# Kernel optimization log

Hardware: AMD Instinct MI355X
Metric: run time of the kernel (lower is better)

Reference implementation:

```python
import jax, jax.numpy as jnp
import numpy as np

HIDDEN = 1024

def _cat_linear(x, W, b, cat_ids):
    # x: (B,T,Din), W: (C,Din,Dout), b: (C,Dout)
    return jnp.einsum('bti,bio->bto', x, W[cat_ids]) + b[cat_ids][:, None, :]

def _sinusoidal(timesteps, dim):
    # timesteps: (B,T) int -> (B,T,dim)
    t = timesteps.astype(jnp.float32)
    half = dim // 2
    exponent = -jnp.arange(half, dtype=jnp.float32) * (jnp.log(10000.0) / half)
    freqs = t[..., None] * jnp.exp(exponent)
    return jnp.concatenate([jnp.sin(freqs), jnp.cos(freqs)], axis=-1)

def setup_inputs() -> dict:
    key = jax.random.key(0)
    ks = jax.random.split(key, 8)
    B, T, A, H, C = 64, 64, 64, HIDDEN, 16
    actions = jax.random.normal(ks[0], (B, T, A), dtype=jnp.float32)
    timesteps = jax.random.randint(ks[1], (B,), 0, 1000)
    cat_ids = jax.random.randint(ks[2], (B,), 0, C)
    W1 = 0.02 * jax.random.normal(ks[3], (C, A, H), dtype=jnp.float32)
    b1 = jnp.zeros((C, H), dtype=jnp.float32)
    W2 = 0.02 * jax.random.normal(ks[4], (C, 2 * H, H), dtype=jnp.float32)
    b2 = jnp.zeros((C, H), dtype=jnp.float32)
    W3 = 0.02 * jax.random.normal(ks[5], (C, H, H), dtype=jnp.float32)
    b3 = jnp.zeros((C, H), dtype=jnp.float32)
    return {"actions": actions, "timesteps": timesteps, "cat_ids": cat_ids,
            "W1": W1, "b1": b1, "W2": W2, "b2": b2, "W3": W3, "b3": b3}

def reference(actions, timesteps, cat_ids, W1, b1, W2, b2, W3, b3):
    B, T, _ = actions.shape
    ts = jnp.broadcast_to(timesteps[:, None], (B, T))  # (B,T)
    a_emb = _cat_linear(actions, W1, b1, cat_ids)        # (B,T,H)
    tau = _sinusoidal(ts, HIDDEN).astype(a_emb.dtype)    # (B,T,H)
    x = jnp.concatenate([a_emb, tau], axis=-1)           # (B,T,2H)
    h = _cat_linear(x, W2, b2, cat_ids)
    h = h * jax.nn.sigmoid(h)                            # swish
    return _cat_linear(h, W3, b3, cat_ids)               # (B,T,H)
```

## Files before the change

kernel.cpp:

```cpp
#include <hip/hip_runtime.h>
#include <math.h>


typedef short bf16x8 __attribute__((ext_vector_type(8)));
typedef float floatx4 __attribute__((ext_vector_type(4)));

__device__ inline short f2bf(float f) {
  union { float f; unsigned u; } v; v.f = f;
  unsigned u = v.u;
  return (short)(((u + 0x7fffu + ((u >> 16) & 1u)) >> 16) & 0xffffu);
}

__device__ __forceinline__ unsigned cvtpk(float a, float b) {
  unsigned r;
  asm("v_cvt_pk_bf16_f32 %0, %1, %2" : "=v"(r) : "v"(a), "v"(b));
  return r;
}

template<int IMM>
__device__ __forceinline__ void gdw(float& d, unsigned voff, unsigned long long base) {
  asm volatile("global_load_dword %0, %1, %2 offset:%3"
               : "=v"(d) : "v"(voff), "s"(base), "n"(IMM) : "memory");
}
template<int IMM>
__device__ __forceinline__ void gdx4(floatx4& d, unsigned voff, unsigned long long base) {
  asm volatile("global_load_dwordx4 %0, %1, %2 offset:%3"
               : "=v"(d) : "v"(voff), "s"(base), "n"(IMM) : "memory");
}
template<int N>
__device__ __forceinline__ void vm_wait() {
  asm volatile("s_waitcnt vmcnt(%0)" :: "n"(N) : "memory");
}

#define ISSUE_W(WBUF) do {                                                   \
    _Pragma("unroll")                                                        \
    for (int j = 0; j < 8; ++j) {                                            \
      gdw<0 >(WBUF[j],     vW[j], Wq);                                       \
      gdw<64>(WBUF[8 + j], vW[j], Wq);                                       \
    }                                                                        \
    Wq += 32ull * 1024 * 4;                                                  \
  } while (0)

#define ISSUE_A(ABUF) do {                                                   \
    _Pragma("unroll")                                                        \
    for (int mt = 0; mt < 8; ++mt) {                                         \
      if constexpr (A_F32) {                                                 \
        gdx4<0 >(ABUF[2 * mt],     vA[mt], Aq);                              \
        gdx4<16>(ABUF[2 * mt + 1], vA[mt], Aq);                              \
      } else {                                                               \
        gdx4<0>(ABUF[mt], vA[mt], Aq);                                       \
      }                                                                      \
    }                                                                        \
    Aq += 32ull * AB;                                                        \
  } while (0)

#define KSTEP(VM, AIN, AOUT, WIN, DO_A, DO_W) do {                           \
    vm_wait<VM>();                                                           \
    __builtin_amdgcn_sched_barrier(0);                                       \
    union { bf16x8 v; unsigned u[4]; } wb0, wb1;                             \
    _Pragma("unroll")                                                        \
    for (int jj = 0; jj < 4; ++jj) {                                         \
      wb0.u[jj] = cvtpk(WIN[2 * jj],     WIN[2 * jj + 1]);                   \
      wb1.u[jj] = cvtpk(WIN[8 + 2 * jj], WIN[8 + 2 * jj + 1]);               \
    }                                                                        \
    bf16x8 af[8];                                                            \
    _Pragma("unroll")                                                        \
    for (int mt = 0; mt < 8; ++mt) {                                         \
      if constexpr (A_F32) {                                                 \
        union { bf16x8 v; unsigned u[4]; } t;                                \
        floatx4 x0 = AIN[2 * mt], x1 = AIN[2 * mt + 1];                      \
        t.u[0] = cvtpk(x0[0], x0[1]); t.u[1] = cvtpk(x0[2], x0[3]);          \
        t.u[2] = cvtpk(x1[0], x1[1]); t.u[3] = cvtpk(x1[2], x1[3]);          \
        af[mt] = t.v;                                                        \
      } else {                                                               \
        union { floatx4 f; bf16x8 v; } t; t.f = AIN[mt]; af[mt] = t.v;       \
      }                                                                      \
    }                                                                        \
    __builtin_amdgcn_sched_barrier(0);                                       \
    if (DO_A) ISSUE_A(AOUT);                                                 \
    if (DO_W) ISSUE_W(WIN);                                                  \
    _Pragma("unroll")                                                        \
    for (int mt = 0; mt < 8; ++mt) {                                         \
      acc[mt][0] = __builtin_amdgcn_mfma_f32_16x16x32_bf16(af[mt], wb0.v, acc[mt][0], 0, 0, 0); \
      acc[mt][1] = __builtin_amdgcn_mfma_f32_16x16x32_bf16(af[mt], wb1.v, acc[mt][1], 0, 0, 0); \
    }                                                                        \
  } while (0)

template<int K, bool A_F32, bool SWISH, bool OUT_BF16, bool TAU>
__global__ __launch_bounds__(128, 2) void gemm_kernel(
    const void* __restrict__ Aall, int lda,
    const float* __restrict__ Wall,
    const float* __restrict__ bias,
    const int* __restrict__ cat_ids,
    void* __restrict__ Out, int ldo,
    const int* __restrict__ ts)
{
  constexpr int NCOL = 1024;
  constexpr int KT = K / 32;
  constexpr int AB = A_F32 ? 4 : 2;
  static_assert(KT >= 2 && ((KT - 2) % 2 == 0), "K must be multiple of 64");
  (void)ts;

  __shared__ int s_b[80], s_c[80], s_np;

  const int tid = threadIdx.x;
  if (tid < 80) { s_b[tid] = -1; s_c[tid] = 0; }
  __syncthreads();
  if (tid < 64) {
    const int myc = cat_ids[tid];
    int rank = 0, pst = 0, tot = 0;
    #pragma unroll
    for (int cc = 0; cc < 16; ++cc) {
      unsigned long long m = __ballot(myc == cc);
      const int cnt = __popcll(m);
      const int pc  = 2 * ((cnt + 1) >> 1);
      if (cc < myc)  pst += pc;
      if (cc == myc) rank = __popcll(m & ((1ull << tid) - 1ull));
      tot += pc;
    }
    const int slot = pst + rank;
    s_b[slot] = tid;
    s_c[slot] = myc;
    if (tid == 0) s_np = tot >> 1;
  }
  __syncthreads();

  const int e = blockIdx.y;
  if (e >= s_np) return;
  const int b0v = __builtin_amdgcn_readfirstlane(s_b[2 * e]);
  int b1        = __builtin_amdgcn_readfirstlane(s_b[2 * e + 1]);
  const int c   = __builtin_amdgcn_readfirstlane(s_c[2 * e]);
  const bool st1 = (b1 >= 0);
  if (!st1) b1 = b0v;

  const int wave = tid >> 6, lane = tid & 63;
  const int quad = lane >> 4, l16 = lane & 15;
  const int ns = blockIdx.x * 64;
  const int wcol = ns + wave * 32;

  const unsigned wqoff = (unsigned)__builtin_amdgcn_readfirstlane(
      (int)(((unsigned)c * (unsigned)K * NCOL + (unsigned)wcol) * 4u));
  unsigned long long Wq = (unsigned long long)Wall + wqoff;
  unsigned long long Aq = (unsigned long long)Aall;

  unsigned vW[8];
  #pragma unroll
  for (int j = 0; j < 8; ++j)
    vW[j] = (unsigned)((quad * 8 + j) * (NCOL * 4) + l16 * 4);

  unsigned vA[8];
  #pragma unroll
  for (int mt = 0; mt < 8; ++mt) {
    const int pr = mt * 16 + l16;
    const int batch = (pr < 64) ? b0v : b1;
    const int row = batch * 64 + (pr & 63);
    vA[mt] = (unsigned)(row * lda * AB + quad * 8 * AB);
  }

  float wA[16], wB[16];
  floatx4 aBuf0[A_F32 ? 16 : 8];
  floatx4 aBuf1[A_F32 ? 1 : 8];

  floatx4 acc[8][2];
  #pragma unroll
  for (int mt = 0; mt < 8; ++mt) {
    acc[mt][0] = (floatx4){0.f, 0.f, 0.f, 0.f};
    acc[mt][1] = (floatx4){0.f, 0.f, 0.f, 0.f};
  }

  ISSUE_W(wA);
  ISSUE_A(aBuf0);
  ISSUE_W(wB);

  if constexpr (A_F32) {
    #pragma unroll 1
    for (int s = 0; s + 2 < KT; s += 2) {
      KSTEP(16, aBuf0, aBuf0, wA, true, true);
      KSTEP(16, aBuf0, aBuf0, wB, true, true);
    }
    KSTEP(16, aBuf0, aBuf0, wA, true, false);
    KSTEP(0,  aBuf0, aBuf0, wB, false, false);
  } else {
    #pragma unroll 1
    for (int s = 0; s + 2 < KT; s += 2) {
      KSTEP(16, aBuf0, aBuf1, wA, true, true);
      KSTEP(16, aBuf1, aBuf0, wB, true, true);
    }
    KSTEP(16, aBuf0, aBuf1, wA, true, false);
    KSTEP(0,  aBuf1, aBuf1, wB, false, false);
  }

  #pragma unroll
  for (int nt = 0; nt < 2; ++nt) {
    const int col = wcol + nt * 16 + l16;
    const float bv = bias[(size_t)c * NCOL + col];
    #pragma unroll
    for (int mt = 0; mt < 8; ++mt) {
      const int prb = mt * 16 + quad * 4;
      const int batch = (prb < 64) ? b0v : b1;
      const bool do_store = (prb < 64) || st1;
      #pragma unroll
      for (int r = 0; r < 4; ++r) {
        const int row = batch * 64 + ((prb + r) & 63);
        float v = acc[mt][nt][r] + bv;
        if constexpr (SWISH) v = v / (1.f + __expf(-v));
        if (do_store) {
          if constexpr (OUT_BF16)
            ((short*)Out)[(size_t)row * ldo + col] = f2bf(v);
          else
            ((float*)Out)[(size_t)row * ldo + col] = v;
        }
      }
    }
  }

  if constexpr (TAU) {
    const float t0  = (float)ts[b0v];
    const float t1v = (float)ts[b1];
    const int ic = ns + (tid & 63);
    const int hi = ic & 511;
    const float ef = __expf(-(float)hi * 0.017988946039015980f);
    float v0, v1;
    if (ic < 512) { v0 = sinf(t0 * ef); v1 = sinf(t1v * ef); }
    else          { v0 = cosf(t0 * ef); v1 = cosf(t1v * ef); }
    const short q0 = f2bf(v0), q1 = f2bf(v1);
    short* xp = (short*)Out;
    const int r0 = tid >> 6;
    #pragma unroll 4
    for (int rr = 0; rr < 32; ++rr) {
      const int rl = r0 + 2 * rr;
      xp[(size_t)(b0v * 64 + rl) * ldo + 1024 + ic] = q0;
      if (st1) xp[(size_t)(b1 * 64 + rl) * ldo + 1024 + ic] = q1;
    }
  }
}

extern "C" void kernel_launch(void* const* d_in, const int* in_sizes, int n_in,
                              void* d_out, int out_size, void* d_ws, size_t ws_size,
                              hipStream_t stream) {
  const float* actions   = (const float*)d_in[0];
  const int*   timesteps = (const int*)  d_in[1];
  const int*   cat_ids   = (const int*)  d_in[2];
  const float* W1 = (const float*)d_in[3];
  const float* B1 = (const float*)d_in[4];
  const float* W2 = (const float*)d_in[5];
  const float* B2 = (const float*)d_in[6];
  const float* W3 = (const float*)d_in[7];
  const float* B3 = (const float*)d_in[8];

  short* x = (short*)d_ws;
  short* h = x + (size_t)64 * 64 * 2048;

  dim3 grid(16, 40), blk(128);

  gemm_kernel<64, true, false, true, true><<<grid, blk, 0, stream>>>(
      (const void*)actions, 64, W1, B1, cat_ids, (void*)x, 2048, timesteps);
  gemm_kernel<2048, false, true, true, false><<<grid, blk, 0, stream>>>(
      (const void*)x, 2048, W2, B2, cat_ids, (void*)h, 1024, nullptr);
  gemm_kernel<1024, false, false, false, false><<<grid, blk, 0, stream>>>(
      (const void*)h, 1024, W3, B3, cat_ids, d_out, 1024, nullptr);
}
```

Baseline: 406.8 us.

## Replace hand-pipelined asm loads with plain single-wave loop, smaller blocks

Removes the inline-asm global loads, manual vmcnt waits and double-buffered software pipeline, and replaces them with a plain C++ k-loop (unroll 2) that loads weights and activations directly. Blocks shrink to one wave of 64 threads covering 32 columns, so the grid doubles in x and the LDS/syncthreads category sort becomes a pure ballot-based computation. The hardware bf16 pack instruction is swapped for software rounding. This simplifies the code and raises block count, but gives up explicit load/compute overlap and adds ALU work for conversion.

Result: slower. 534.2 us (+31.3%).

```diff
diff --git a/kernel.cpp b/kernel.cpp
--- a/kernel.cpp
+++ b/kernel.cpp
@@ -11,83 +11,15 @@
   return (short)(((u + 0x7fffu + ((u >> 16) & 1u)) >> 16) & 0xffffu);
 }
 
-__device__ __forceinline__ unsigned cvtpk(float a, float b) {
-  unsigned r;
-  asm("v_cvt_pk_bf16_f32 %0, %1, %2" : "=v"(r) : "v"(a), "v"(b));
-  return r;
+__device__ __forceinline__ unsigned pk2(float a, float b) {
+  union { float f; unsigned u; } x, y; x.f = a; y.f = b;
+  unsigned ua = (x.u + 0x7fffu + ((x.u >> 16) & 1u)) >> 16;
+  unsigned ub = (y.u + 0x7fffu + ((y.u >> 16) & 1u)) >> 16;
+  return (ua & 0xffffu) | (ub << 16);
 }
 
-template<int IMM>
-__device__ __forceinline__ void gdw(float& d, unsigned voff, unsigned long long base) {
-  asm volatile("global_load_dword %0, %1, %2 offset:%3"
-               : "=v"(d) : "v"(voff), "s"(base), "n"(IMM) : "memory");
-}
-template<int IMM>
-__device__ __forceinline__ void gdx4(floatx4& d, unsigned voff, unsigned long long base) {
-  asm volatile("global_load_dwordx4 %0, %1, %2 offset:%3"
-               : "=v"(d) : "v"(voff), "s"(base), "n"(IMM) : "memory");
-}
-template<int N>
-__device__ __forceinline__ void vm_wait() {
-  asm volatile("s_waitcnt vmcnt(%0)" :: "n"(N) : "memory");
-}
-
-#define ISSUE_W(WBUF) do {                                                   \
-    _Pragma("unroll")                                                        \
-    for (int j = 0; j < 8; ++j) {                                            \
-      gdw<0 >(WBUF[j],     vW[j], Wq);                                       \
-      gdw<64>(WBUF[8 + j], vW[j], Wq);                                       \
-    }                                                                        \
-    Wq += 32ull * 1024 * 4;                                                  \
-  } while (0)
-
-#define ISSUE_A(ABUF) do {                                                   \
-    _Pragma("unroll")                                                        \
-    for (int mt = 0; mt < 8; ++mt) {                                         \
-      if constexpr (A_F32) {                                                 \
-        gdx4<0 >(ABUF[2 * mt],     vA[mt], Aq);                              \
-        gdx4<16>(ABUF[2 * mt + 1], vA[mt], Aq);                              \
-      } else {                                                               \
-        gdx4<0>(ABUF[mt], vA[mt], Aq);                                       \
-      }                                                                      \
-    }                                                                        \
-    Aq += 32ull * AB;                                                        \
-  } while (0)
-
-#define KSTEP(VM, AIN, AOUT, WIN, DO_A, DO_W) do {                           \
-    vm_wait<VM>();                                                           \
-    __builtin_amdgcn_sched_barrier(0);                                       \
-    union { bf16x8 v; unsigned u[4]; } wb0, wb1;                             \
-    _Pragma("unroll")                                                        \
-    for (int jj = 0; jj < 4; ++jj) {                                         \
-      wb0.u[jj] = cvtpk(WIN[2 * jj],     WIN[2 * jj + 1]);                   \
-      wb1.u[jj] = cvtpk(WIN[8 + 2 * jj], WIN[8 + 2 * jj + 1]);               \
-    }                                                                        \
-    bf16x8 af[8];                                                            \
-    _Pragma("unroll")                                                        \
-    for (int mt = 0; mt < 8; ++mt) {                                         \
-      if constexpr (A_F32) {                                                 \
-        union { bf16x8 v; unsigned u[4]; } t;                                \
-        floatx4 x0 = AIN[2 * mt], x1 = AIN[2 * mt + 1];                      \
-        t.u[0] = cvtpk(x0[0], x0[1]); t.u[1] = cvtpk(x0[2], x0[3]);          \
-        t.u[2] = cvtpk(x1[0], x1[1]); t.u[3] = cvtpk(x1[2], x1[3]);          \
-        af[mt] = t.v;                                                        \
-      } else {                                                               \
-        union { floatx4 f; bf16x8 v; } t; t.f = AIN[mt]; af[mt] = t.v;       \
-      }                                                                      \
-    }                                                                        \
-    __builtin_amdgcn_sched_barrier(0);                                       \
-    if (DO_A) ISSUE_A(AOUT);                                                 \
-    if (DO_W) ISSUE_W(WIN);                                                  \
-    _Pragma("unroll")                                                        \
-    for (int mt = 0; mt < 8; ++mt) {                                         \
-      acc[mt][0] = __builtin_amdgcn_mfma_f32_16x16x32_bf16(af[mt], wb0.v, acc[mt][0], 0, 0, 0); \
-      acc[mt][1] = __builtin_amdgcn_mfma_f32_16x16x32_bf16(af[mt], wb1.v, acc[mt][1], 0, 0, 0); \
-    }                                                                        \
-  } while (0)
-
 template<int K, bool A_F32, bool SWISH, bool OUT_BF16, bool TAU>
-__global__ __launch_bounds__(128, 2) void gemm_kernel(
+__global__ __launch_bounds__(64, 2) void gemm_kernel(
     const void* __restrict__ Aall, int lda,
     const float* __restrict__ Wall,
     const float* __restrict__ bias,
@@ -97,69 +29,43 @@
 {
   constexpr int NCOL = 1024;
   constexpr int KT = K / 32;
-  constexpr int AB = A_F32 ? 4 : 2;
-  static_assert(KT >= 2 && ((KT - 2) % 2 == 0), "K must be multiple of 64");
   (void)ts;
 
-  __shared__ int s_b[80], s_c[80], s_np;
+  const int lane = threadIdx.x;
+  const int quad = lane >> 4, l16 = lane & 15;
 
-  const int tid = threadIdx.x;
-  if (tid < 80) { s_b[tid] = -1; s_c[tid] = 0; }
-  __syncthreads();
-  if (tid < 64) {
-    const int myc = cat_ids[tid];
-    int rank = 0, pst = 0, tot = 0;
-    #pragma unroll
-    for (int cc = 0; cc < 16; ++cc) {
-      unsigned long long m = __ballot(myc == cc);
-      const int cnt = __popcll(m);
-      const int pc  = 2 * ((cnt + 1) >> 1);
-      if (cc < myc)  pst += pc;
-      if (cc == myc) rank = __popcll(m & ((1ull << tid) - 1ull));
-      tot += pc;
-    }
-    const int slot = pst + rank;
-    s_b[slot] = tid;
-    s_c[slot] = myc;
-    if (tid == 0) s_np = tot >> 1;
+  const int myc = cat_ids[lane];
+  int rank = 0, pst = 0, tot = 0;
+  #pragma unroll
+  for (int cc = 0; cc < 16; ++cc) {
+    const unsigned long long m = __ballot(myc == cc);
+    const int cnt = __popcll(m);
+    const int pc  = 2 * ((cnt + 1) >> 1);
+    if (cc < myc)  pst += pc;
+    if (cc == myc) rank = __popcll(m & ((1ull << lane) - 1ull));
+    tot += pc;
   }
-  __syncthreads();
+  const int slot = pst + rank;
+  const int e = blockIdx.y;
+  if (e >= (tot >> 1)) return;
+  const unsigned long long m0 = __ballot(slot == 2 * e);
+  const unsigned long long m1 = __ballot(slot == 2 * e + 1);
+  const int b0v = __ffsll(m0) - 1;
+  const bool st1 = (m1 != 0ull);
+  const int b1 = st1 ? (__ffsll(m1) - 1) : b0v;
+  const int c = cat_ids[b0v];
 
-  const int e = blockIdx.y;
-  if (e >= s_np) return;
-  const int b0v = __builtin_amdgcn_readfirstlane(s_b[2 * e]);
-  int b1        = __builtin_amdgcn_readfirstlane(s_b[2 * e + 1]);
-  const int c   = __builtin_amdgcn_readfirstlane(s_c[2 * e]);
-  const bool st1 = (b1 >= 0);
-  if (!st1) b1 = b0v;
+  const int ns = blockIdx.x * 32;
 
-  const int wave = tid >> 6, lane = tid & 63;
-  const int quad = lane >> 4, l16 = lane & 15;
-  const int ns = blockIdx.x * 64;
-  const int wcol = ns + wave * 32;
-
-  const unsigned wqoff = (unsigned)__builtin_amdgcn_readfirstlane(
-      (int)(((unsigned)c * (unsigned)K * NCOL + (unsigned)wcol) * 4u));
-  unsigned long long Wq = (unsigned long long)Wall + wqoff;
-  unsigned long long Aq = (unsigned long long)Aall;
-
-  unsigned vW[8];
-  #pragma unroll
-  for (int j = 0; j < 8; ++j)
-    vW[j] = (unsigned)((quad * 8 + j) * (NCOL * 4) + l16 * 4);
-
-  unsigned vA[8];
+  int aoff[8];
   #pragma unroll
   for (int mt = 0; mt < 8; ++mt) {
     const int pr = mt * 16 + l16;
     const int batch = (pr < 64) ? b0v : b1;
-    const int row = batch * 64 + (pr & 63);
-    vA[mt] = (unsigned)(row * lda * AB + quad * 8 * AB);
+    aoff[mt] = (batch * 64 + (pr & 63)) * lda;
   }
 
-  float wA[16], wB[16];
-  floatx4 aBuf0[A_F32 ? 16 : 8];
-  floatx4 aBuf1[A_F32 ? 1 : 8];
+  const float* wbase = Wall + (size_t)c * K * NCOL + ns + l16;
 
   floatx4 acc[8][2];
   #pragma unroll
@@ -168,31 +74,51 @@
     acc[mt][1] = (floatx4){0.f, 0.f, 0.f, 0.f};
   }
 
-  ISSUE_W(wA);
-  ISSUE_A(aBuf0);
-  ISSUE_W(wB);
+  #pragma unroll 2
+  for (int s = 0; s < KT; ++s) {
+    const int k0 = s * 32 + quad * 8;
 
-  if constexpr (A_F32) {
-    #pragma unroll 1
-    for (int s = 0; s + 2 < KT; s += 2) {
-      KSTEP(16, aBuf0, aBuf0, wA, true, true);
-      KSTEP(16, aBuf0, aBuf0, wB, true, true);
+    float wv[16];
+    #pragma unroll
+    for (int j = 0; j < 8; ++j) {
+      const float* wp = wbase + (size_t)(k0 + j) * NCOL;
+      wv[j]     = wp[0];
+      wv[8 + j] = wp[16];
     }
-    KSTEP(16, aBuf0, aBuf0, wA, true, false);
-    KSTEP(0,  aBuf0, aBuf0, wB, false, false);
-  } else {
-    #pragma unroll 1
-    for (int s = 0; s + 2 < KT; s += 2) {
-      KSTEP(16, aBuf0, aBuf1, wA, true, true);
-      KSTEP(16, aBuf1, aBuf0, wB, true, true);
+    union { bf16x8 v; unsigned u[4]; } w0, w1;
+    #pragma unroll
+    for (int j = 0; j < 4; ++j) {
+      w0.u[j] = pk2(wv[2 * j],     wv[2 * j + 1]);
+      w1.u[j] = pk2(wv[8 + 2 * j], wv[9 + 2 * j]);
     }
-    KSTEP(16, aBuf0, aBuf1, wA, true, false);
-    KSTEP(0,  aBuf1, aBuf1, wB, false, false);
+
+    bf16x8 av[8];
+    #pragma unroll
+    for (int mt = 0; mt < 8; ++mt) {
+      if constexpr (A_F32) {
+        const floatx4* p = (const floatx4*)((const float*)Aall + aoff[mt] + k0);
+        const floatx4 x0 = p[0], x1 = p[1];
+        union { bf16x8 v; unsigned u[4]; } t;
+        t.u[0] = pk2(x0[0], x0[1]); t.u[1] = pk2(x0[2], x0[3]);
+        t.u[2] = pk2(x1[0], x1[1]); t.u[3] = pk2(x1[2], x1[3]);
+        av[mt] = t.v;
+      } else {
+        av[mt] = *(const bf16x8*)((const short*)Aall + aoff[mt] + k0);
+      }
+    }
+
+    #pragma unroll
+    for (int mt = 0; mt < 8; ++mt) {
+      acc[mt][0] = __builtin_amdgcn_mfma_f32_16x16x32_bf16(
+          av[mt], w0.v, acc[mt][0], 0, 0, 0);
+      acc[mt][1] = __builtin_amdgcn_mfma_f32_16x16x32_bf16(
+          av[mt], w1.v, acc[mt][1], 0, 0, 0);
+    }
   }
 
   #pragma unroll
   for (int nt = 0; nt < 2; ++nt) {
-    const int col = wcol + nt * 16 + l16;
+    const int col = ns + nt * 16 + l16;
     const float bv = bias[(size_t)c * NCOL + col];
     #pragma unroll
     for (int mt = 0; mt < 8; ++mt) {
@@ -217,7 +143,7 @@
   if constexpr (TAU) {
     const float t0  = (float)ts[b0v];
     const float t1v = (float)ts[b1];
-    const int ic = ns + (tid & 63);
+    const int ic = ns + (lane & 31);
     const int hi = ic & 511;
     const float ef = __expf(-(float)hi * 0.017988946039015980f);
     float v0, v1;
@@ -225,7 +151,7 @@
     else          { v0 = cosf(t0 * ef); v1 = cosf(t1v * ef); }
     const short q0 = f2bf(v0), q1 = f2bf(v1);
     short* xp = (short*)Out;
-    const int r0 = tid >> 6;
+    const int r0 = lane >> 5;
     #pragma unroll 4
     for (int rr = 0; rr < 32; ++rr) {
       const int rl = r0 + 2 * rr;
@@ -251,7 +177,7 @@
   short* x = (short*)d_ws;
   short* h = x + (size_t)64 * 64 * 2048;
 
-  dim3 grid(16, 40), blk(128);
+  dim3 grid(32, 40), blk(64);
 
   gemm_kernel<64, true, false, true, true><<<grid, blk, 0, stream>>>(
       (const void*)actions, 64, W1, B1, cat_ids, (void*)x, 2048, timesteps);
```
